# Kernel optimization log

Hardware: AMD Instinct MI355X
Metric: run time of the kernel (lower is better)

## Reference

```python
import jax, jax.numpy as jnp
import numpy as np

BATCH, SEQ, INPUT_SIZE, RESERVOIR = 32, 2048, 256, 512


def setup_inputs() -> dict:
    key = jax.random.key(0)
    k_x, k_w, k_d = jax.random.split(key, 3)
    x = jax.random.normal(k_x, (BATCH, SEQ, INPUT_SIZE), dtype=jnp.float32)
    # input_projection weight: uniform(-1, 1), shape [R, input_size]
    W_in = jax.random.uniform(k_w, (RESERVOIR, INPUT_SIZE), dtype=jnp.float32, minval=-1.0, maxval=1.0)
    # diagonal of state_projection: uniform(-0.5, 0.5)
    d = jax.random.uniform(k_d, (RESERVOIR,), dtype=jnp.float32, minval=-0.5, maxval=0.5)
    return {"x": x, "W_in": W_in, "d": d}


def reference(x, W_in, d):
    B, T, _ = x.shape
    R = d.shape[0]
    # input projection: [B, T, R]
    u = jnp.einsum('bti,ri->btr', x, W_in)

    # recurrence: state_t = tanh(d * state_{t-1} + u_t)  (leak gate is dead code: 0*old + 1*new)
    # torch loop fills indices 1..T-1 of all_states (T+1 slots), then returns [:, 1:],
    # so the final returned timestep is all zeros.
    def step(state, u_t):
        new_state = jnp.tanh(d * state + u_t)
        return new_state, new_state

    init = jnp.zeros((B, R), dtype=x.dtype)
    u_tm = jnp.swapaxes(u[:, 1:, :], 0, 1)  # time-major [T-1, B, R]
    _, states = jax.lax.scan(step, init, u_tm)
    states = jnp.swapaxes(states, 0, 1)  # [B, T-1, R]
    tail = jnp.zeros((B, 1, R), dtype=x.dtype)
    return jnp.concatenate([states, tail], axis=1)  # [B, T, R]
```

## Files before the change

### kernel.cpp

```cpp
#include <hip/hip_runtime.h>

#define BATCH 32
#define SEQT  2048
#define INSZ  256
#define RSV   512
#define MTOT  (BATCH * SEQT)
#define BM 128
#define BN 128
#define BK 32
#define NK  (INSZ / BK)
#define LSA 40
#define ASTR 1040
#define LOPLANE 131072

#define K2LOG2E 2.8853900817779268f

using f16x8 = __attribute__((ext_vector_type(8))) _Float16;
using f16x4 = __attribute__((ext_vector_type(4))) _Float16;
using f32x4 = __attribute__((ext_vector_type(4))) float;

typedef __attribute__((address_space(1))) unsigned int as1_u32;
typedef __attribute__((address_space(3))) unsigned int as3_u32;
#define GLDS16(gp, lp) __builtin_amdgcn_global_load_lds((as1_u32*)(gp), (as3_u32*)(lp), 16, 0, 0)

static __device__ __forceinline__ float esn_step(float s, float u, float dK) {
    float z  = __builtin_fmaf(dK, s, u * K2LOG2E);
    float e  = __builtin_amdgcn_exp2f(z);
    float rc = __builtin_amdgcn_rcpf(1.0f + e);
    return __builtin_fmaf(-2.0f, rc, 1.0f);
}


__global__ __launch_bounds__(256) void esn_convw(const float* __restrict__ W,
                                                 _Float16* __restrict__ W16T) {
    const int i = blockIdx.x * 256 + threadIdx.x;
    const int bn = i >> 12, ks = (i >> 9) & 7, c = i & 511;
    const int q = c >> 7, row = c & 127;
    const float* src = W + (size_t)(bn * 128 + row) * INSZ + ks * 32 + q * 8;
    float4 v0 = *(const float4*)src;
    float4 v1 = *(const float4*)(src + 4);
    float w8[8] = {v0.x, v0.y, v0.z, v0.w, v1.x, v1.y, v1.z, v1.w};
    f16x8 h, l;
    #pragma unroll
    for (int j = 0; j < 8; ++j) {
        _Float16 hh = (_Float16)w8[j];
        h[j] = hh;
        l[j] = (_Float16)(w8[j] - (float)hh);
    }
    *(f16x8*)(W16T + (size_t)i * 8) = h;
    *(f16x8*)(W16T + LOPLANE + (size_t)i * 8) = l;
}

__global__ __launch_bounds__(256) void esn_gemm_f(const float* __restrict__ X,
                                                  const _Float16* __restrict__ W16T,
                                                  _Float16* __restrict__ U16) {
    __shared__ _Float16 Ash[2][4 * ASTR];
    __shared__ _Float16 Bh[2][4096];
    __shared__ _Float16 Bl[2][4096];

    const int tid  = threadIdx.x;
    const int lane = tid & 63;
    const int wid  = tid >> 6;
    const int wr   = wid >> 1, wc = wid & 1;
    const int lgc = (blockIdx.x & 7) * 256 + (blockIdx.x >> 3);
    const int bm = lgc >> 2, bn = lgc & 3;

    const int srow = tid >> 3;
    const int scol = (tid & 7) * 4;
    const int qa   = scol >> 3;
    const int ha   = (scol >> 2) & 1;

    f32x4 acc[4][4] = {};

    #pragma unroll
    for (int j = 0; j < 2; ++j) {
        const int cb = (wid * 2 + j) * 64;
        const _Float16* gh = W16T + ((size_t)(bn * 8 + 0) * 512 + cb + lane) * 8;
        GLDS16(gh, &Bh[0][cb * 8]);
        GLDS16(gh + LOPLANE, &Bl[0][cb * 8]);
    }
    #pragma unroll
    for (int p = 0; p < 4; ++p) {
        const int row = srow + p * 32;
        float4 av = *(const float4*)(X + (size_t)(bm * BM + row) * INSZ + scol);
        float a4[4] = {av.x, av.y, av.z, av.w};
        f16x4 ah;
        #pragma unroll
        for (int j = 0; j < 4; ++j) ah[j] = (_Float16)a4[j];
        *(f16x4*)&Ash[0][qa * ASTR + row * 8 + ha * 4] = ah;
    }
    __syncthreads();

    #pragma unroll
    for (int ks = 0; ks < NK; ++ks) {
        const int cur = ks & 1, nxt = cur ^ 1;
        float4 xr[4];
        if (ks + 1 < NK) {
            #pragma unroll
            for (int j = 0; j < 2; ++j) {
                const int cb = (wid * 2 + j) * 64;
                const _Float16* gh = W16T + ((size_t)(bn * 8 + ks + 1) * 512 + cb + lane) * 8;
                GLDS16(gh, &Bh[nxt][cb * 8]);
                GLDS16(gh + LOPLANE, &Bl[nxt][cb * 8]);
            }
            #pragma unroll
            for (int p = 0; p < 4; ++p) {
                const int row = srow + p * 32;
                xr[p] = *(const float4*)(X + (size_t)(bm * BM + row) * INSZ + (ks + 1) * BK + scol);
            }
        }

        f16x8 af[4], bfh[4], bfl[4];
        const int qf = lane >> 4;
        #pragma unroll
        for (int m = 0; m < 4; ++m)
            af[m] = *(const f16x8*)&Ash[cur][qf * ASTR + (wr * 64 + m * 16 + (lane & 15)) * 8];
        #pragma unroll
        for (int n = 0; n < 4; ++n) {
            const int rr = qf * 1024 + (wc * 64 + n * 16 + (lane & 15)) * 8;
            bfh[n] = *(const f16x8*)&Bh[cur][rr];
            bfl[n] = *(const f16x8*)&Bl[cur][rr];
        }
        #pragma unroll
        for (int m = 0; m < 4; ++m)
            #pragma unroll
            for (int n = 0; n < 4; ++n) {
                acc[m][n] = __builtin_amdgcn_mfma_f32_16x16x32_f16(bfh[n], af[m], acc[m][n], 0, 0, 0);
                acc[m][n] = __builtin_amdgcn_mfma_f32_16x16x32_f16(bfl[n], af[m], acc[m][n], 0, 0, 0);
            }

        if (ks + 1 < NK) {
            #pragma unroll
            for (int p = 0; p < 4; ++p) {
                const int row = srow + p * 32;
                float a4[4] = {xr[p].x, xr[p].y, xr[p].z, xr[p].w};
                f16x4 ah;
                #pragma unroll
                for (int j = 0; j < 4; ++j) ah[j] = (_Float16)a4[j];
                *(f16x4*)&Ash[nxt][qa * ASTR + row * 8 + ha * 4] = ah;
            }
        }
        __syncthreads();
    }

    #pragma unroll
    for (int m = 0; m < 4; ++m) {
        const int gm = bm * BM + wr * 64 + m * 16 + (lane & 15);
        #pragma unroll
        for (int n = 0; n < 4; ++n) {
            const int gr = bn * BN + wc * 64 + n * 16 + (lane >> 4) * 4;
            f16x4 o;
            #pragma unroll
            for (int j = 0; j < 4; ++j) o[j] = (_Float16)acc[m][n][j];
            *(f16x4*)(U16 + (size_t)gm * RSV + gr) = o;
        }
    }
}

__global__ __launch_bounds__(256) void esn_recur_f(const _Float16* __restrict__ U16,
                                                   const float* __restrict__ D,
                                                   float* __restrict__ OUT) {
    const int tid  = threadIdx.x;
    const int b    = blockIdx.x >> 4;
    const int seg  = (blockIdx.x >> 1) & 7;
    const int half = blockIdx.x & 1;
    const int r    = half * 256 + tid;

    const _Float16* ub = U16 + (size_t)b * SEQT * RSV + r;
    float* ob = OUT + (size_t)b * SEQT * RSV + r;
    const float dK = D[r] * K2LOG2E;
    const int t0 = seg * 256;

    float s = 0.0f;
    if (seg) {
        #pragma unroll 8
        for (int k = 0; k < 32; ++k)
            s = esn_step(s, (float)ub[(size_t)(t0 - 31 + k) * RSV], dK);
    }

    _Float16 bufA[8], bufB[8];
    #pragma unroll
    for (int j = 0; j < 8; ++j) bufA[j] = ub[(size_t)(t0 + 1 + j) * RSV];
    #pragma unroll
    for (int j = 0; j < 8; ++j) bufB[j] = ub[(size_t)(t0 + 9 + j) * RSV];

#define PROC8F(buf, tt) do {                                  \
    _Pragma("unroll")                                         \
    for (int j = 0; j < 8; ++j) {                             \
        s = esn_step(s, (float)buf[j], dK);                   \
        ob[(size_t)((tt) + j) * RSV] = s;                     \
        int idx = (tt) + j + 17;                              \
        idx = idx < SEQT ? idx : SEQT - 1;                    \
        buf[j] = ub[(size_t)idx * RSV];                       \
    }                                                         \
} while (0)

    int t = t0;
    for (int it = 0; it < 16; ++it) {
        PROC8F(bufA, t);
        PROC8F(bufB, t + 8);
        t += 16;
    }
#undef PROC8F
    if (seg == 7) ob[(size_t)(SEQT - 1) * RSV] = 0.0f;
}


__global__ __launch_bounds__(256) void esn_gemm_fb(const float* __restrict__ X,
                                                   const float* __restrict__ W,
                                                   float* __restrict__ U) {
    __shared__ _Float16 Ash[128 * LSA];
    __shared__ _Float16 Bsh[128 * 72];

    const int tid  = threadIdx.x;
    const int lane = tid & 63;
    const int wid  = tid >> 6;
    const int wr   = wid >> 1, wc = wid & 1;
    const int bm   = blockIdx.x >> 2, bn = blockIdx.x & 3;
    const int srow = tid >> 3;
    const int scol = (tid & 7) * 4;

    f32x4 acc[4][4] = {};

    for (int ks = 0; ks < NK; ++ks) {
        __syncthreads();
        #pragma unroll
        for (int p = 0; p < 4; ++p) {
            const int row = srow + p * 32;
            float4 av = *(const float4*)(X + (size_t)(bm * 128 + row) * INSZ + ks * 32 + scol);
            float4 bv = *(const float4*)(W + (size_t)(bn * 128 + row) * INSZ + ks * 32 + scol);
            float a4[4] = {av.x, av.y, av.z, av.w};
            float b4[4] = {bv.x, bv.y, bv.z, bv.w};
            f16x4 ah, bh, bl;
            #pragma unroll
            for (int j = 0; j < 4; ++j) {
                ah[j] = (_Float16)a4[j];
                _Float16 h = (_Float16)b4[j];
                bh[j] = h;
                bl[j] = (_Float16)(b4[j] - (float)h);
            }
            *(f16x4*)&Ash[row * LSA + scol] = ah;
            *(f16x4*)&Bsh[row * 72 + scol] = bh;
            *(f16x4*)&Bsh[row * 72 + 32 + scol] = bl;
        }
        __syncthreads();

        f16x8 af[4], bfh[4], bfl[4];
        #pragma unroll
        for (int m = 0; m < 4; ++m)
            af[m] = *(const f16x8*)&Ash[(wr * 64 + m * 16 + (lane & 15)) * LSA + (lane >> 4) * 8];
        #pragma unroll
        for (int n = 0; n < 4; ++n) {
            const _Float16* p = &Bsh[(wc * 64 + n * 16 + (lane & 15)) * 72 + (lane >> 4) * 8];
            bfh[n] = *(const f16x8*)p;
            bfl[n] = *(const f16x8*)(p + 32);
        }
        #pragma unroll
        for (int m = 0; m < 4; ++m)
            #pragma unroll
            for (int n = 0; n < 4; ++n) {
                acc[m][n] = __builtin_amdgcn_mfma_f32_16x16x32_f16(af[m], bfh[n], acc[m][n], 0, 0, 0);
                acc[m][n] = __builtin_amdgcn_mfma_f32_16x16x32_f16(af[m], bfl[n], acc[m][n], 0, 0, 0);
            }
    }

    #pragma unroll
    for (int m = 0; m < 4; ++m) {
        const int row = bm * 128 + wr * 64 + m * 16 + (lane >> 4) * 4;
        #pragma unroll
        for (int n = 0; n < 4; ++n) {
            const int col = bn * 128 + wc * 64 + n * 16 + (lane & 15);
            f32x4 v = acc[m][n];
            #pragma unroll
            for (int j = 0; j < 4; ++j)
                U[(size_t)(row + j) * RSV + col] = v[j];
        }
    }
}

__global__ __launch_bounds__(64) void esn_recur_fb(float* __restrict__ OUT,
                                                   const float* __restrict__ D) {
    const int gid = blockIdx.x * 64 + threadIdx.x;
    const int b = gid >> 9;
    const int r = gid & (RSV - 1);
    float* base = OUT + (size_t)b * SEQT * RSV + r;
    const float dK = D[r] * K2LOG2E;
    float s = 0.0f;

    float bA[8], bB[8], bC[8], bD[8];
    #pragma unroll
    for (int j = 0; j < 8; ++j) bA[j] = base[(size_t)(1 + j) * RSV];
    #pragma unroll
    for (int j = 0; j < 8; ++j) bB[j] = base[(size_t)(9 + j) * RSV];
    #pragma unroll
    for (int j = 0; j < 8; ++j) bC[j] = base[(size_t)(17 + j) * RSV];
    #pragma unroll
    for (int j = 0; j < 8; ++j) bD[j] = base[(size_t)(25 + j) * RSV];

#define PROC8B(buf, tt) do {                                  \
    _Pragma("unroll")                                         \
    for (int j = 0; j < 8; ++j) {                             \
        s = esn_step(s, buf[j], dK);                          \
        base[(size_t)((tt) + j) * RSV] = s;                   \
        int idx = (tt) + 33 + j;                              \
        idx = idx < SEQT ? idx : SEQT - 1;                    \
        buf[j] = base[(size_t)idx * RSV];                     \
    }                                                         \
} while (0)

    int t = 0;
    for (int it = 0; it < 63; ++it) {
        PROC8B(bA, t);
        PROC8B(bB, t + 8);
        PROC8B(bC, t + 16);
        PROC8B(bD, t + 24);
        t += 32;
    }
#undef PROC8B
    #pragma unroll
    for (int j = 0; j < 8; ++j) { s = esn_step(s, bA[j], dK); base[(size_t)(2016 + j) * RSV] = s; }
    #pragma unroll
    for (int j = 0; j < 8; ++j) { s = esn_step(s, bB[j], dK); base[(size_t)(2024 + j) * RSV] = s; }
    #pragma unroll
    for (int j = 0; j < 8; ++j) { s = esn_step(s, bC[j], dK); base[(size_t)(2032 + j) * RSV] = s; }
    #pragma unroll
    for (int j = 0; j < 7; ++j) { s = esn_step(s, bD[j], dK); base[(size_t)(2040 + j) * RSV] = s; }

    base[(size_t)(SEQT - 1) * RSV] = 0.0f;
}

extern "C" void kernel_launch(void* const* d_in, const int* in_sizes, int n_in,
                              void* d_out, int out_size, void* d_ws, size_t ws_size,
                              hipStream_t stream) {
    const float* X = (const float*)d_in[0];
    const float* W = (const float*)d_in[1];
    const float* D = (const float*)d_in[2];
    float* OUT = (float*)d_out;

    const size_t W16T_BYTES = (size_t)2 * RSV * INSZ * sizeof(_Float16);
    const size_t U16_BYTES  = (size_t)MTOT * RSV * sizeof(_Float16);
    if (ws_size >= W16T_BYTES + U16_BYTES) {
        _Float16* W16T = (_Float16*)d_ws;
        _Float16* U16  = (_Float16*)((char*)d_ws + W16T_BYTES);
        esn_convw<<<dim3(64), dim3(256), 0, stream>>>(W, W16T);
        esn_gemm_f<<<dim3((MTOT / BM) * (RSV / BN)), dim3(256), 0, stream>>>(X, W16T, U16);
        esn_recur_f<<<dim3(BATCH * 8 * 2), dim3(256), 0, stream>>>(U16, D, OUT);
    } else {
        esn_gemm_fb<<<dim3((MTOT / 128) * (RSV / 128)), dim3(256), 0, stream>>>(X, W, OUT);
        esn_recur_fb<<<dim3(BATCH * RSV / 64), dim3(64), 0, stream>>>(OUT, D);
    }
}
```

Before: 271.6 us.

## Pre-convert X to fp16 tiled layout and split recurrence into more segments

Adds a separate kernel that converts X to fp16 in an MFMA-friendly tiled layout. The GEMM can then load A through direct global-to-LDS copies, drops double buffering and caps occupancy via launch bounds. The recurrence now uses 16 segments of 128 steps instead of 8 of 256, doubling parallelism while adding more warm-up overhead. The extra conversion pass costs an additional read of X (fp32) and a write and read of the fp16 copy.

```diff
diff --git a/kernel.cpp b/kernel.cpp
--- a/kernel.cpp
+++ b/kernel.cpp
@@ -10,8 +10,7 @@
 #define BK 32
 #define NK  (INSZ / BK)
 #define LSA 40
-#define ASTR 1040
-#define LOPLANE 131072
+#define WLOPL 131072
 
 #define K2LOG2E 2.8853900817779268f
 
@@ -48,15 +47,33 @@
         l[j] = (_Float16)(w8[j] - (float)hh);
     }
     *(f16x8*)(W16T + (size_t)i * 8) = h;
-    *(f16x8*)(W16T + LOPLANE + (size_t)i * 8) = l;
-}
-
-__global__ __launch_bounds__(256) void esn_gemm_f(const float* __restrict__ X,
-                                                  const _Float16* __restrict__ W16T,
-                                                  _Float16* __restrict__ U16) {
-    __shared__ _Float16 Ash[2][4 * ASTR];
-    __shared__ _Float16 Bh[2][4096];
-    __shared__ _Float16 Bl[2][4096];
+    *(f16x8*)(W16T + WLOPL + (size_t)i * 8) = l;
+}
+
+__global__ __launch_bounds__(256) void esn_convx(const float* __restrict__ X,
+                                                 _Float16* __restrict__ X16T) {
+    const int i = blockIdx.x * 256 + threadIdx.x;
+    const int bm = i >> 10, ks = (i >> 7) & 7, row = i & 127;
+    const float* src = X + (size_t)(bm * 128 + row) * INSZ + ks * 32;
+    _Float16* dst = X16T + ((size_t)(bm * 8 + ks) * 512 + row) * 8;
+    #pragma unroll
+    for (int q = 0; q < 4; ++q) {
+        float4 v0 = *(const float4*)(src + q * 8);
+        float4 v1 = *(const float4*)(src + q * 8 + 4);
+        float w8[8] = {v0.x, v0.y, v0.z, v0.w, v1.x, v1.y, v1.z, v1.w};
+        f16x8 h;
+        #pragma unroll
+        for (int j = 0; j < 8; ++j) h[j] = (_Float16)w8[j];
+        *(f16x8*)(dst + (size_t)q * 128 * 8) = h;
+    }
+}
+
+__global__ __launch_bounds__(256, 5) void esn_gemm_f(const _Float16* __restrict__ X16T,
+                                                     const _Float16* __restrict__ W16T,
+                                                     _Float16* __restrict__ U16) {
+    __shared__ _Float16 Ash[4096];
+    __shared__ _Float16 Bh[4096];
+    __shared__ _Float16 Bl[4096];
 
     const int tid  = threadIdx.x;
     const int lane = tid & 63;
@@ -65,61 +82,31 @@
     const int lgc = (blockIdx.x & 7) * 256 + (blockIdx.x >> 3);
     const int bm = lgc >> 2, bn = lgc & 3;
 
-    const int srow = tid >> 3;
-    const int scol = (tid & 7) * 4;
-    const int qa   = scol >> 3;
-    const int ha   = (scol >> 2) & 1;
-
     f32x4 acc[4][4] = {};
 
-    #pragma unroll
-    for (int j = 0; j < 2; ++j) {
-        const int cb = (wid * 2 + j) * 64;
-        const _Float16* gh = W16T + ((size_t)(bn * 8 + 0) * 512 + cb + lane) * 8;
-        GLDS16(gh, &Bh[0][cb * 8]);
-        GLDS16(gh + LOPLANE, &Bl[0][cb * 8]);
-    }
-    #pragma unroll
-    for (int p = 0; p < 4; ++p) {
-        const int row = srow + p * 32;
-        float4 av = *(const float4*)(X + (size_t)(bm * BM + row) * INSZ + scol);
-        float a4[4] = {av.x, av.y, av.z, av.w};
-        f16x4 ah;
-        #pragma unroll
-        for (int j = 0; j < 4; ++j) ah[j] = (_Float16)a4[j];
-        *(f16x4*)&Ash[0][qa * ASTR + row * 8 + ha * 4] = ah;
-    }
-    __syncthreads();
-
-    #pragma unroll
     for (int ks = 0; ks < NK; ++ks) {
-        const int cur = ks & 1, nxt = cur ^ 1;
-        float4 xr[4];
-        if (ks + 1 < NK) {
-            #pragma unroll
-            for (int j = 0; j < 2; ++j) {
-                const int cb = (wid * 2 + j) * 64;
-                const _Float16* gh = W16T + ((size_t)(bn * 8 + ks + 1) * 512 + cb + lane) * 8;
-                GLDS16(gh, &Bh[nxt][cb * 8]);
-                GLDS16(gh + LOPLANE, &Bl[nxt][cb * 8]);
-            }
-            #pragma unroll
-            for (int p = 0; p < 4; ++p) {
-                const int row = srow + p * 32;
-                xr[p] = *(const float4*)(X + (size_t)(bm * BM + row) * INSZ + (ks + 1) * BK + scol);
-            }
-        }
+        __syncthreads();
+        #pragma unroll
+        for (int j = 0; j < 2; ++j) {
+            const int cb = (wid * 2 + j) * 64;
+            const _Float16* ga = X16T + ((size_t)(bm * 8 + ks) * 512 + cb + lane) * 8;
+            const _Float16* gw = W16T + ((size_t)(bn * 8 + ks) * 512 + cb + lane) * 8;
+            GLDS16(ga, &Ash[cb * 8]);
+            GLDS16(gw, &Bh[cb * 8]);
+            GLDS16(gw + WLOPL, &Bl[cb * 8]);
+        }
+        __syncthreads();
 
         f16x8 af[4], bfh[4], bfl[4];
         const int qf = lane >> 4;
         #pragma unroll
         for (int m = 0; m < 4; ++m)
-            af[m] = *(const f16x8*)&Ash[cur][qf * ASTR + (wr * 64 + m * 16 + (lane & 15)) * 8];
+            af[m] = *(const f16x8*)&Ash[(qf * 128 + wr * 64 + m * 16 + (lane & 15)) * 8];
         #pragma unroll
         for (int n = 0; n < 4; ++n) {
-            const int rr = qf * 1024 + (wc * 64 + n * 16 + (lane & 15)) * 8;
-            bfh[n] = *(const f16x8*)&Bh[cur][rr];
-            bfl[n] = *(const f16x8*)&Bl[cur][rr];
+            const int rr = (qf * 128 + wc * 64 + n * 16 + (lane & 15)) * 8;
+            bfh[n] = *(const f16x8*)&Bh[rr];
+            bfl[n] = *(const f16x8*)&Bl[rr];
         }
         #pragma unroll
         for (int m = 0; m < 4; ++m)
@@ -128,19 +115,6 @@
                 acc[m][n] = __builtin_amdgcn_mfma_f32_16x16x32_f16(bfh[n], af[m], acc[m][n], 0, 0, 0);
                 acc[m][n] = __builtin_amdgcn_mfma_f32_16x16x32_f16(bfl[n], af[m], acc[m][n], 0, 0, 0);
             }
-
-        if (ks + 1 < NK) {
-            #pragma unroll
-            for (int p = 0; p < 4; ++p) {
-                const int row = srow + p * 32;
-                float a4[4] = {xr[p].x, xr[p].y, xr[p].z, xr[p].w};
-                f16x4 ah;
-                #pragma unroll
-                for (int j = 0; j < 4; ++j) ah[j] = (_Float16)a4[j];
-                *(f16x4*)&Ash[nxt][qa * ASTR + row * 8 + ha * 4] = ah;
-            }
-        }
-        __syncthreads();
     }
 
     #pragma unroll
@@ -161,15 +135,15 @@
                                                    const float* __restrict__ D,
                                                    float* __restrict__ OUT) {
     const int tid  = threadIdx.x;
-    const int b    = blockIdx.x >> 4;
-    const int seg  = (blockIdx.x >> 1) & 7;
+    const int b    = blockIdx.x >> 5;
+    const int seg  = (blockIdx.x >> 1) & 15;
     const int half = blockIdx.x & 1;
     const int r    = half * 256 + tid;
 
     const _Float16* ub = U16 + (size_t)b * SEQT * RSV + r;
     float* ob = OUT + (size_t)b * SEQT * RSV + r;
     const float dK = D[r] * K2LOG2E;
-    const int t0 = seg * 256;
+    const int t0 = seg * 128;
 
     float s = 0.0f;
     if (seg) {
@@ -196,13 +170,13 @@
 } while (0)
 
     int t = t0;
-    for (int it = 0; it < 16; ++it) {
+    for (int it = 0; it < 8; ++it) {
         PROC8F(bufA, t);
         PROC8F(bufB, t + 8);
         t += 16;
     }
 #undef PROC8F
-    if (seg == 7) ob[(size_t)(SEQT - 1) * RSV] = 0.0f;
+    if (seg == 15) ob[(size_t)(SEQT - 1) * RSV] = 0.0f;
 }
 
 
@@ -338,13 +312,16 @@
     float* OUT = (float*)d_out;
 
     const size_t W16T_BYTES = (size_t)2 * RSV * INSZ * sizeof(_Float16);
+    const size_t X16T_BYTES = (size_t)MTOT * INSZ * sizeof(_Float16);
     const size_t U16_BYTES  = (size_t)MTOT * RSV * sizeof(_Float16);
-    if (ws_size >= W16T_BYTES + U16_BYTES) {
+    if (ws_size >= W16T_BYTES + X16T_BYTES + U16_BYTES) {
         _Float16* W16T = (_Float16*)d_ws;
-        _Float16* U16  = (_Float16*)((char*)d_ws + W16T_BYTES);
+        _Float16* X16T = (_Float16*)((char*)d_ws + W16T_BYTES);
+        _Float16* U16  = (_Float16*)((char*)d_ws + W16T_BYTES + X16T_BYTES);
         esn_convw<<<dim3(64), dim3(256), 0, stream>>>(W, W16T);
-        esn_gemm_f<<<dim3((MTOT / BM) * (RSV / BN)), dim3(256), 0, stream>>>(X, W16T, U16);
-        esn_recur_f<<<dim3(BATCH * 8 * 2), dim3(256), 0, stream>>>(U16, D, OUT);
+        esn_convx<<<dim3(2048), dim3(256), 0, stream>>>(X, X16T);
+        esn_gemm_f<<<dim3((MTOT / BM) * (RSV / BN)), dim3(256), 0, stream>>>(X16T, W16T, U16);
+        esn_recur_f<<<dim3(BATCH * 16 * 2), dim3(256), 0, stream>>>(U16, D, OUT);
     } else {
         esn_gemm_fb<<<dim3((MTOT / 128) * (RSV / 128)), dim3(256), 0, stream>>>(X, W, OUT);
         esn_recur_fb<<<dim3(BATCH * RSV / 64), dim3(64), 0, stream>>>(OUT, D);
```

Measured after the change: 339.0 us. +24.8%, slower.
